# Optimization experiments

Hardware: AMD Instinct MI355X
Metric: run time of the kernel (lower is better)

The kernel has to match this reference:

```python
import jax, jax.numpy as jnp
import numpy as np

D0, D1 = 512, 512          # PSF / sensor dims (DIMS0, DIMS1)
P0, P1 = D0 // 2, D1 // 2  # pad sizes
ITERS = 20
MU1, MU2, MU3 = 1e-6, 1e-5, 1e-5
TAU = 1e-4 * 1000.0        # 0.1, as in module


def _ct(x):  # zero-pad crop-adjoint: sensor -> full size
    return jnp.pad(x, [(0, 0)] * (x.ndim - 2) + [(P0, P0), (P1, P1)])


def _c(x):  # crop full -> sensor size
    return x[..., P0:P0 + D0, P1:P1 + D1]


def _fft2(x):
    return jnp.fft.fft2(x, axes=(-2, -1))


def _ifft2(x):
    return jnp.fft.ifft2(x, axes=(-2, -1))


def _ifftshift(x):
    return jnp.fft.ifftshift(x, axes=(-2, -1))


def _fftshift(x):
    return jnp.fft.fftshift(x, axes=(-2, -1))


def _H(x, Hf):  # forward blur operator
    return jnp.real(_fftshift(_ifft2(Hf * _fft2(_ifftshift(x)))))


def _Hadj(x, Hf):  # adjoint blur operator
    return jnp.real(_fftshift(_ifft2(jnp.conj(Hf) * _fft2(_ifftshift(x)))))


def _psi(x):  # finite differences stacked on last axis -> (..., 2)
    return jnp.stack([jnp.roll(x, 1, axis=-2) - x,
                      jnp.roll(x, 1, axis=-1) - x], axis=-1)


def _psit(u):  # adjoint of _psi
    d0, d1 = u[..., 0], u[..., 1]
    return (jnp.roll(d0, -1, axis=-2) - d0) + (jnp.roll(d1, -1, axis=-1) - d1)


def _soft(v, thresh):
    return jnp.sign(v) * jnp.maximum(jnp.abs(v) - thresh, 0.0)


def _make_ltl():  # FFT of laplacian kernel (Psi^T Psi in Fourier domain)
    lapl = np.zeros((2 * D0, 2 * D1), np.float32)
    lapl[0, 0] = 4.0
    lapl[0, 1] = -1.0
    lapl[1, 0] = -1.0
    lapl[0, -1] = -1.0
    lapl[-1, 0] = -1.0
    return jnp.fft.fft2(jnp.asarray(lapl))


def setup_inputs() -> dict:
    key = jax.random.key(0)
    k1, k2 = jax.random.split(key)
    y = jax.random.uniform(k1, (8, 1, D0, D1), dtype=jnp.float32)
    h = jax.random.uniform(k2, (D0, D1), dtype=jnp.float32)
    return {"y": y, "h": h}


def reference(y, h):
    Hf = _fft2(_ifftshift(_ct(h[None])))            # (1, 2D0, 2D1) complex
    LtL = _make_ltl()                               # (2D0, 2D1) complex
    Vdiv = 1.0 / (_ct(jnp.ones((1, 1, D0, D1), y.dtype)) + MU1)
    Rdiv = 1.0 / (MU1 * jnp.abs(jnp.conj(Hf) * Hf) + MU2 * jnp.abs(LtL) + MU3)
    CTy = _ct(y)                                    # (B,1,2D0,2D1)

    B = y.shape[0]
    full = (B, 1, 2 * D0, 2 * D1)
    X = jnp.zeros(full, y.dtype)
    U = jnp.zeros(full + (2,), y.dtype)
    V = jnp.zeros(full, y.dtype)
    W = jnp.zeros(full, y.dtype)
    a1 = jnp.zeros(full, y.dtype)
    a2 = jnp.zeros(full + (2,), y.dtype)
    a3 = jnp.zeros(full, y.dtype)

    def step(carry, _):
        X, U, V, W, a1, a2, a3 = carry
        U = _soft(_psi(X) + a2 / MU2, TAU / MU2)
        V = Vdiv * (a1 + MU1 * _H(X, Hf) + CTy)
        W = jnp.maximum(a3 / MU3 + X, 0.0)
        r = (MU3 * W - a3) + _psit(MU2 * U - a2) + _Hadj(MU1 * V - a1, Hf)
        X = jnp.real(_fftshift(_ifft2(Rdiv * _fft2(_ifftshift(r)))))
        a1 = a1 + MU1 * (_H(X, Hf) - V)
        a2 = a2 + MU2 * (_psi(X) - U)
        a3 = a3 + MU3 * (X - W)
        return (X, U, V, W, a1, a2, a3), None

    (X, _, _, _, _, _, _), _ = jax.lax.scan(step, (X, U, V, W, a1, a2, a3), None, length=ITERS)
    return _c(X)
```

## Files before the change

kernel.cpp:

```cpp
#include <hip/hip_runtime.h>
#include <math.h>

#define N 1024
#define NN (1024*1024)
#define BATCH 8

static constexpr float MU1 = 1e-6f, MU2 = 1e-5f, MU3 = 1e-5f;

__device__ __forceinline__ float2 cmulf(float2 a, float2 b){
  return make_float2(a.x*b.x - a.y*b.y, a.x*b.y + a.y*b.x);
}
__device__ __forceinline__ float2 conjf(float2 a){ return make_float2(a.x, -a.y); }
__device__ __forceinline__ float softf(float v, float T){
  float a = fmaxf(fabsf(v) - T, 0.f);
  return copysignf(a, v);
}
__device__ __forceinline__ int rev4_10(int p){
  return ((p&3)<<8) | (((p>>2)&3)<<6) | (((p>>4)&3)<<4) | (((p>>6)&3)<<2) | ((p>>8)&3);
}
__device__ __forceinline__ int foldc(int k){
  if (k == 0) return 0;
  if (k == 512) return 1;
  return (k < 512) ? 2*k : 2*(1024-k)+1;
}
__device__ __forceinline__ int unfoldc(int c){
  if (c < 2) return c ? 512 : 0;
  return (c & 1) ? 1024 - ((c-1)>>1) : (c>>1);
}

#define BF4F(x0,x1,x2,x3,u0,u1,u2,u3) { \
  float2 t02p = make_float2((x0).x+(x2).x, (x0).y+(x2).y); \
  float2 t02m = make_float2((x0).x-(x2).x, (x0).y-(x2).y); \
  float2 t13p = make_float2((x1).x+(x3).x, (x1).y+(x3).y); \
  float2 t13m = make_float2((x1).x-(x3).x, (x1).y-(x3).y); \
  u0 = make_float2(t02p.x+t13p.x, t02p.y+t13p.y); \
  u2 = make_float2(t02p.x-t13p.x, t02p.y-t13p.y); \
  u1 = make_float2(t02m.x+t13m.y, t02m.y-t13m.x); \
  u3 = make_float2(t02m.x-t13m.y, t02m.y+t13m.x); }
#define BF4I(x0,x1,x2,x3,u0,u1,u2,u3) { \
  float2 t02p = make_float2((x0).x+(x2).x, (x0).y+(x2).y); \
  float2 t02m = make_float2((x0).x-(x2).x, (x0).y-(x2).y); \
  float2 t13p = make_float2((x1).x+(x3).x, (x1).y+(x3).y); \
  float2 t13m = make_float2((x1).x-(x3).x, (x1).y-(x3).y); \
  u0 = make_float2(t02p.x+t13p.x, t02p.y+t13p.y); \
  u2 = make_float2(t02p.x-t13p.x, t02p.y-t13p.y); \
  u1 = make_float2(t02m.x-t13m.y, t02m.y+t13m.x); \
  u3 = make_float2(t02m.x+t13m.y, t02m.y-t13m.x); }

template<int DIR>
__device__ __forceinline__ void fft1024(float2* bufA, float2* bufB,
                                        const float2* Ws, int tid){
  float2* cur = bufA; float2* oth = bufB;
  int s = 1;
  for (int st = 0; st < 10; ++st){
    int m = 512 >> st;
    #pragma unroll
    for (int bb = 0; bb < 2; ++bb){
      int b = tid + bb*256;
      int p = b >> st;
      int q = b & (s-1);
      float2 a = cur[b];
      float2 c = cur[b + 512];
      float2 w = Ws[b & ~(s-1)];
      if (DIR > 0) w.y = -w.y;
      float2 d = make_float2(a.x - c.x, a.y - c.y);
      oth[q + s*(2*p)]   = make_float2(a.x + c.x, a.y + c.y);
      oth[q + s*(2*p+1)] = cmulf(d, w);
    }
    __syncthreads();
    float2* t = cur; cur = oth; oth = t;
    s <<= 1;
  }
}

__global__ void k_twiddle(float2* W){
  int j = blockIdx.x*blockDim.x + threadIdx.x;
  if (j < 768){
    double a = -2.0 * M_PI * (double)j / 1024.0;
    W[j] = make_float2((float)cos(a), (float)sin(a));
  }
}

__global__ void k_build_h(const float* __restrict__ h, float2* __restrict__ Z){
  int idx = blockIdx.x*256 + threadIdx.x;
  int i = idx >> 10, j = idx & 1023;
  float v = 0.f;
  if (i >= 256 && i < 768 && j >= 256 && j < 768)
    v = h[(i-256)*512 + (j-256)];
  Z[idx] = make_float2(v, 0.f);
}

__global__ void k_filters2(const float2* __restrict__ ZT, float2* __restrict__ HfCb,
                           float* __restrict__ RdCb){
  int id = blockIdx.x*256 + threadIdx.x;
  int blk = id >> 13;
  int rem = id & 8191;
  int p = rem >> 3, c = rem & 7;
  int colp = (blk << 3) | c;
  int ki = rev4_10(p);
  int kj = unfoldc(colp);
  float2 v = ZT[((size_t)kj << 10) | (size_t)ki];
  float sgn = ((ki + kj) & 1) ? -1.f : 1.f;
  HfCb[id] = make_float2(sgn*v.x, sgn*v.y);
  double mag2 = (double)v.x*(double)v.x + (double)v.y*(double)v.y;
  double ltl = 4.0 - 2.0*cos(2.0*M_PI*(double)ki/1024.0)
                   - 2.0*cos(2.0*M_PI*(double)kj/1024.0);
  double rd = 1.0 / ((double)MU1*mag2 + (double)MU2*ltl + (double)MU3);
  RdCb[id] = (float)(rd / ((double)N * (double)N));
}

__global__ void k_init(float* __restrict__ X, float* __restrict__ G1,
                       float* __restrict__ K, float* __restrict__ M,
                       float* __restrict__ G0a, float* __restrict__ G0b,
                       const float* __restrict__ y){
  int idx = blockIdx.x*256 + threadIdx.x;
  int e = idx >> 20, r = (idx >> 10) & 1023, c = idx & 1023;
  X[idx] = 0.f; G1[idx] = 0.f; K[idx] = 0.f; G0a[idx] = 0.f; G0b[idx] = 0.f;
  float m = 0.f;
  if (r >= 256 && r < 768 && c >= 256 && c < 768)
    m = y[(size_t)e*262144 + (size_t)(r-256)*512 + (c-256)] * (MU1/(1.f + MU1));
  M[idx] = m;
}

__global__ __launch_bounds__(256) void k_pA(const float* __restrict__ X,
                                            const float* __restrict__ G0r,
                                            float* __restrict__ G0w,
                                            const float* __restrict__ G1,
                                            const float* __restrict__ K,
                                            const float* __restrict__ M,
                                            float2* __restrict__ Z,
                                            const float2* __restrict__ Wg, int e0){
  __shared__ float2 bufA[N], bufB[N], Ws[512];
  int tid = threadIdx.x;
  int bid = blockIdx.x;
  int i = ((bid & 7) << 7) + (bid >> 3);
  int ce = blockIdx.y, e = e0 + ce;
  size_t eb  = (size_t)e*NN;
  size_t rb  = eb + (size_t)i*N;
  size_t rbm = eb + (size_t)((i-1)&1023)*N;
  size_t rbp = eb + (size_t)((i+1)&1023)*N;
  size_t zb  = (size_t)ce*NN + (size_t)i*N;
  for (int k = tid; k < 512; k += 256) Ws[k] = Wg[k];
  const float T = 1e4f;
  for (int j = tid; j < N; j += 256){
    float xm = X[rbm+j], x = X[rb+j], xp = X[rbp+j];
    float psi0  = xm - x;
    float psi0p = x - xp;
    float g0  = G0r[rb+j], g0p = G0r[rbp+j];
    float u0  = softf(2.f*psi0  - g0 *(1.f/MU2), T);
    float u0p = softf(2.f*psi0p - g0p*(1.f/MU2), T);
    float g0n  = MU2*(u0  - psi0 ) + g0;
    float g0np = MU2*(u0p - psi0p) + g0p;
    G0w[rb+j] = g0n;
    int jp = (j+1) & 1023;
    float s = K[rb+j] + (g0np - g0n) + (G1[rb+jp] - G1[rb+j]);
    bufA[j] = make_float2(s, M[rb+j]);
  }
  __syncthreads();
  fft1024<-1>(bufA, bufB, Ws, tid);
  for (int j = tid; j < N; j += 256) bufB[foldc(j)] = bufA[j];
  __syncthreads();
  for (int j = tid; j < N; j += 256) Z[zb+j] = bufB[j];
}

template<int DIR>
__global__ __launch_bounds__(256) void k_fft_row(float2* Z, const float2* __restrict__ Wg){
  __shared__ float2 bufA[N], bufB[N], Ws[512];
  int tid = threadIdx.x;
  size_t base = ((size_t)blockIdx.y * N + blockIdx.x) * N;
  for (int k = tid; k < 512; k += 256) Ws[k] = Wg[k];
  for (int k = tid; k < N; k += 256) bufA[k] = Z[base + k];
  __syncthreads();
  fft1024<DIR>(bufA, bufB, Ws, tid);
  for (int k = tid; k < N; k += 256) Z[base + k] = bufA[k];
}

__global__ void k_transpose_ip(float2* Z){
  __shared__ float2 ta[32][33], tb[32][33];
  int t = blockIdx.x, ti = 0;
  while (t >= 32 - ti){ t -= 32 - ti; ti++; }
  int tj = ti + t;
  size_t base = (size_t)blockIdx.y * NN;
  int ra = ti*32, ca = tj*32;
  for (int k = threadIdx.y; k < 32; k += 8){
    ta[k][threadIdx.x] = Z[base + (size_t)(ra+k)*N + ca + threadIdx.x];
    if (ti != tj)
      tb[k][threadIdx.x] = Z[base + (size_t)(ca+k)*N + ra + threadIdx.x];
  }
  __syncthreads();
  for (int k = threadIdx.y; k < 32; k += 8){
    Z[base + (size_t)(ra+k)*N + ca + threadIdx.x] = (ti!=tj) ? tb[threadIdx.x][k]
                                                             : ta[threadIdx.x][k];
    if (ti != tj)
      Z[base + (size_t)(ca+k)*N + ra + threadIdx.x] = ta[threadIdx.x][k];
  }
}

#define TADDR(r,c) ((((r)*9) + (c)) ^ (((r) & 16) >> 1))
#define CPV 512
__global__ __launch_bounds__(CPV, 4) void k_colpass(float2* __restrict__ Z,
    const float2* __restrict__ HfCb, const float* __restrict__ RdCb,
    const float2* __restrict__ Wg){
  __shared__ float2 tile[9216];
  __shared__ float2 Ws[768];
  int tid = threadIdx.x;
  int blk = blockIdx.x;
  size_t zbase = (size_t)blockIdx.y*NN + ((size_t)blk<<3);
  for (int k = tid; k < 768; k += CPV) Ws[k] = Wg[k];
  for (int k = tid; k < 8192; k += CPV){
    int r = k >> 3, c = k & 7;
    tile[TADDR(r,c)] = Z[zbase + (size_t)r*N + c];
  }
  __syncthreads();
  {
    int c = tid & 7, j2 = tid >> 3;
    float2 v[4][4];
    #pragma unroll
    for (int a = 0; a < 4; ++a)
      #pragma unroll
      for (int b = 0; b < 4; ++b)
        v[a][b] = tile[TADDR(j2 + 64*b + 256*a, c)];
    #pragma unroll
    for (int b = 0; b < 4; ++b){
      int j1 = j2 + 64*b;
      float2 u0,u1,u2,u3;
      BF4F(v[0][b],v[1][b],v[2][b],v[3][b],u0,u1,u2,u3);
      v[0][b] = u0;
      v[1][b] = cmulf(u1, Ws[j1]);
      v[2][b] = cmulf(u2, Ws[2*j1]);
      v[3][b] = cmulf(u3, Ws[3*j1]);
    }
    int tw = j2 << 2;
    #pragma unroll
    for (int a = 0; a < 4; ++a){
      float2 u0,u1,u2,u3;
      BF4F(v[a][0],v[a][1],v[a][2],v[a][3],u0,u1,u2,u3);
      tile[TADDR(j2 + 256*a, c)]       = u0;
      tile[TADDR(j2 + 64 + 256*a, c)]  = cmulf(u1, Ws[tw]);
      tile[TADDR(j2 + 128 + 256*a, c)] = cmulf(u2, Ws[2*tw]);
      tile[TADDR(j2 + 192 + 256*a, c)] = cmulf(u3, Ws[3*tw]);
    }
  }
  __syncthreads();
  {
    int c = tid & 7, vv = tid >> 3;
    int B2 = vv >> 2, j2 = vv & 3;
    int r0 = 64*B2 + j2;
    float2 v[4][4];
    #pragma unroll
    for (int a = 0; a < 4; ++a)
      #pragma unroll
      for (int b = 0; b < 4; ++b)
        v[a][b] = tile[TADDR(r0 + 4*b + 16*a, c)];
    #pragma unroll
    for (int b = 0; b < 4; ++b){
      int tw = (j2 + 4*b) << 4;
      float2 u0,u1,u2,u3;
      BF4F(v[0][b],v[1][b],v[2][b],v[3][b],u0,u1,u2,u3);
      v[0][b] = u0;
      v[1][b] = cmulf(u1, Ws[tw]);
      v[2][b] = cmulf(u2, Ws[2*tw]);
      v[3][b] = cmulf(u3, Ws[3*tw]);
    }
    int tw3 = j2 << 6;
    #pragma unroll
    for (int a = 0; a < 4; ++a){
      float2 u0,u1,u2,u3;
      BF4F(v[a][0],v[a][1],v[a][2],v[a][3],u0,u1,u2,u3);
      tile[TADDR(r0 + 16*a, c)]      = u0;
      tile[TADDR(r0 + 16*a + 4, c)]  = cmulf(u1, Ws[tw3]);
      tile[TADDR(r0 + 16*a + 8, c)]  = cmulf(u2, Ws[2*tw3]);
      tile[TADDR(r0 + 16*a + 12, c)] = cmulf(u3, Ws[3*tw3]);
    }
  }
  __syncthreads();
  for (int k = tid; k < 2048; k += CPV){
    int c = k & 7, t = k >> 3;
    int r = 4*t;
    float2 x0 = tile[TADDR(r,c)],   x1 = tile[TADDR(r+1,c)];
    float2 x2 = tile[TADDR(r+2,c)], x3 = tile[TADDR(r+3,c)];
    float2 u0,u1,u2,u3;
    BF4F(x0,x1,x2,x3,u0,u1,u2,u3);
    tile[TADDR(r,c)] = u0; tile[TADDR(r+1,c)] = u1;
    tile[TADDR(r+2,c)] = u2; tile[TADDR(r+3,c)] = u3;
  }
  __syncthreads();
  {
    size_t fbase = (size_t)blk << 13;
    for (int k = tid; k < 8192; k += CPV){
      int p = k >> 3, c = k & 7;
      int k1 = rev4_10(p);
      int q = rev4_10((1024 - k1) & 1023);
      int colp = (blk << 3) + c;
      int cm = (colp < 2) ? c : (c ^ 1);
      int pid = (q << 3) | cm;
      if (pid < k) continue;
      float2 Zk = tile[TADDR(p,c)];
      float2 Zr = tile[TADDR(q,cm)];
      float Sre = 0.5f*(Zk.x + Zr.x);
      float Sim = 0.5f*(Zk.y - Zr.y);
      float Mre = 0.5f*(Zk.y + Zr.y);
      float Mim = 0.5f*(Zr.x - Zk.x);
      float2 hf = HfCb[fbase + k];
      float rd  = RdCb[fbase + k];
      float fr = rd*(Sre + hf.x*Mre + hf.y*Mim);
      float fi = rd*(Sim + hf.x*Mim - hf.y*Mre);
      float hr = hf.x*fr - hf.y*fi;
      float hi = hf.x*fi + hf.y*fr;
      tile[TADDR(p,c)] = make_float2(fr - hi, fi + hr);
      if (pid != k) tile[TADDR(q,cm)] = make_float2(fr + hi, hr - fi);
    }
  }
  __syncthreads();
  {
    int c = tid & 7, G = tid >> 3;
    int r0 = 16*G;
    float2 v[4][4];
    #pragma unroll
    for (int a = 0; a < 4; ++a)
      #pragma unroll
      for (int b = 0; b < 4; ++b)
        v[a][b] = tile[TADDR(r0 + 4*a + b, c)];
    #pragma unroll
    for (int a = 0; a < 4; ++a){
      float2 u0,u1,u2,u3;
      BF4I(v[a][0],v[a][1],v[a][2],v[a][3],u0,u1,u2,u3);
      v[a][0]=u0; v[a][1]=u1; v[a][2]=u2; v[a][3]=u3;
    }
    #pragma unroll
    for (int b = 0; b < 4; ++b){
      int tw = b << 6;
      float2 x0 = v[0][b];
      float2 x1 = cmulf(v[1][b], conjf(Ws[tw]));
      float2 x2 = cmulf(v[2][b], conjf(Ws[2*tw]));
      float2 x3 = cmulf(v[3][b], conjf(Ws[3*tw]));
      float2 u0,u1,u2,u3;
      BF4I(x0,x1,x2,x3,u0,u1,u2,u3);
      tile[TADDR(r0 + b, c)]      = u0;
      tile[TADDR(r0 + 4 + b, c)]  = u1;
      tile[TADDR(r0 + 8 + b, c)]  = u2;
      tile[TADDR(r0 + 12 + b, c)] = u3;
    }
  }
  __syncthreads();
  {
    int c = tid & 7, vv = tid >> 3;
    int T3 = vv >> 4, jj = vv & 15;
    int r0 = 256*T3 + jj;
    float2 v[4][4];
    #pragma unroll
    for (int a = 0; a < 4; ++a)
      #pragma unroll
      for (int b = 0; b < 4; ++b)
        v[a][b] = tile[TADDR(r0 + 16*a + 64*b, c)];
    int tw2 = jj << 4;
    #pragma unroll
    for (int b = 0; b < 4; ++b){
      float2 x0 = v[0][b];
      float2 x1 = cmulf(v[1][b], conjf(Ws[tw2]));
      float2 x2 = cmulf(v[2][b], conjf(Ws[2*tw2]));
      float2 x3 = cmulf(v[3][b], conjf(Ws[3*tw2]));
      float2 u0,u1,u2,u3;
      BF4I(x0,x1,x2,x3,u0,u1,u2,u3);
      v[0][b]=u0; v[1][b]=u1; v[2][b]=u2; v[3][b]=u3;
    }
    #pragma unroll
    for (int a = 0; a < 4; ++a){
      int tw = (jj + 16*a) << 2;
      float2 x0 = v[a][0];
      float2 x1 = cmulf(v[a][1], conjf(Ws[tw]));
      float2 x2 = cmulf(v[a][2], conjf(Ws[2*tw]));
      float2 x3 = cmulf(v[a][3], conjf(Ws[3*tw]));
      float2 u0,u1,u2,u3;
      BF4I(x0,x1,x2,x3,u0,u1,u2,u3);
      tile[TADDR(r0 + 16*a, c)]       = u0;
      tile[TADDR(r0 + 16*a + 64, c)]  = u1;
      tile[TADDR(r0 + 16*a + 128, c)] = u2;
      tile[TADDR(r0 + 16*a + 192, c)] = u3;
    }
  }
  __syncthreads();
  for (int k = tid; k < 2048; k += CPV){
    int c = k & 7, t = k >> 3;
    float2 x0 = tile[TADDR(t,c)];
    float2 x1 = cmulf(tile[TADDR(t+256,c)], conjf(Ws[t]));
    float2 x2 = cmulf(tile[TADDR(t+512,c)], conjf(Ws[2*t]));
    float2 x3 = cmulf(tile[TADDR(t+768,c)], conjf(Ws[3*t]));
    float2 u0,u1,u2,u3;
    BF4I(x0,x1,x2,x3,u0,u1,u2,u3);
    tile[TADDR(t,c)] = u0;     tile[TADDR(t+256,c)] = u1;
    tile[TADDR(t+512,c)] = u2; tile[TADDR(t+768,c)] = u3;
  }
  __syncthreads();
  for (int k = tid; k < 8192; k += CPV){
    int r = k >> 3, c = k & 7;
    Z[zbase + (size_t)r*N + c] = tile[TADDR(r,c)];
  }
}

__global__ __launch_bounds__(256) void k_p5(const float2* __restrict__ Z,
                                            float* __restrict__ X, float* __restrict__ K,
                                            float* __restrict__ M, float* __restrict__ G1,
                                            const float* __restrict__ y,
                                            float* __restrict__ out, int writeOut,
                                            const float2* __restrict__ Wg, int e0){
  __shared__ float2 bufA[N], bufB[N], Ws[512];
  int tid = threadIdx.x;
  int i = blockIdx.x, ce = blockIdx.y, e = e0 + ce;
  size_t zb = (size_t)ce*NN + (size_t)i*N;
  size_t sb = (size_t)e*NN + (size_t)i*N;
  for (int k = tid; k < 512; k += 256) Ws[k] = Wg[k];
  for (int k = tid; k < N; k += 256) bufB[k] = Z[zb + k];
  __syncthreads();
  for (int k = tid; k < N; k += 256) bufA[k] = bufB[foldc(k)];
  __syncthreads();
  fft1024<1>(bufA, bufB, Ws, tid);
  bool rcent = (i >= 256 && i < 768);
  const float T = 1e4f;
  for (int j = tid; j < N; j += 256){
    float x = bufA[j].x, hx = bufA[j].y;
    X[sb+j] = x;
    float kk = K[sb+j];
    float w = fmaxf(2.f*x - kk*(1.f/MU3), 0.f);
    K[sb+j] = MU3*(w - x) + kk;
    float m = M[sb+j];
    bool cent = rcent && (j >= 256 && j < 768);
    float cty  = cent ? y[(size_t)e*262144 + (size_t)(i-256)*512 + (j-256)] : 0.f;
    float vdiv = cent ? (1.f/(1.f + MU1)) : (1.f/MU1);
    float v = vdiv*(2.f*MU1*hx - m + cty);
    M[sb+j] = MU1*(v - hx) + m;
    float xm = bufA[(j-1)&1023].x;
    float psi1 = xm - x;
    float g1 = G1[sb+j];
    float u1 = softf(2.f*psi1 - g1*(1.f/MU2), T);
    G1[sb+j] = MU2*(u1 - psi1) + g1;
    if (writeOut && cent)
      out[(size_t)e*262144 + (size_t)(i-256)*512 + (j-256)] = x;
  }
}

__global__ void k_crop(const float* __restrict__ X, float* __restrict__ out){
  int t = blockIdx.x*256 + threadIdx.x;
  int e = t >> 18;
  int r = (t >> 9) & 511;
  int c = t & 511;
  out[t] = X[(size_t)e*NN + (size_t)(r+256)*N + (c+256)];
}

extern "C" void kernel_launch(void* const* d_in, const int* in_sizes, int n_in,
                              void* d_out, int out_size, void* d_ws, size_t ws_size,
                              hipStream_t stream){
  const float* y = (const float*)d_in[0];
  const float* h = (const float*)d_in[1];
  float* out = (float*)d_out;

  size_t fplane = (size_t)BATCH * NN;
  float* X   = (float*)d_ws;
  float* G1  = X   + fplane;
  float* K   = G1  + fplane;
  float* M   = K   + fplane;
  float* G0a = M   + fplane;
  float* G0b = G0a + fplane;
  float2* HfCb = (float2*)(G0b + fplane);
  float*  RdCb = (float*)(HfCb + NN);
  float2* Wtab = (float2*)(RdCb + NN);
  float2* Zws  = Wtab + 768;
  size_t used = (size_t)((char*)Zws - (char*)d_ws);

  int CH = 0;
  for (int c = BATCH; c >= 1; c >>= 1)
    if (used + (size_t)c * NN * sizeof(float2) <= ws_size){ CH = c; break; }
  bool fallback = (CH == 0);
  float2* Z = fallback ? (float2*)d_out : Zws;
  if (CH == 0) CH = 1;

  k_twiddle<<<3, 256, 0, stream>>>(Wtab);
  k_build_h<<<NN/256, 256, 0, stream>>>(h, Z);
  k_fft_row<-1><<<dim3(N,1), 256, 0, stream>>>(Z, Wtab);
  k_transpose_ip<<<dim3(528,1), dim3(32,8), 0, stream>>>(Z);
  k_fft_row<-1><<<dim3(N,1), 256, 0, stream>>>(Z, Wtab);
  k_filters2<<<NN/256, 256, 0, stream>>>(Z, HfCb, RdCb);
  k_init<<<BATCH*NN/256, 256, 0, stream>>>(X, G1, K, M, G0a, G0b, y);

  for (int t = 0; t < 20; ++t){
    const float* G0r = (t & 1) ? G0b : G0a;
    float*       G0w = (t & 1) ? G0a : G0b;
    int wo = (t == 19 && !fallback) ? 1 : 0;
    for (int e0 = 0; e0 < BATCH; e0 += CH){
      k_pA<<<dim3(N,CH), 256, 0, stream>>>(X, G0r, G0w, G1, K, M, Z, Wtab, e0);
      k_colpass<<<dim3(128,CH), CPV, 0, stream>>>(Z, HfCb, RdCb, Wtab);
      k_p5<<<dim3(N,CH), 256, 0, stream>>>(Z, X, K, M, G1, y, out, wo, Wtab, e0);
    }
  }
  if (fallback)
    k_crop<<<(BATCH*512*512)/256, 256, 0, stream>>>(X, out);
}
```

Measured before the change: 3.769 ms.

## Use radix-4 row FFTs, on-chip twiddles and Rdiv, skip init pass

Replaces the radix-2 ping-pong row FFTs in the forward and final passes with in-place radix-4 FFTs on a padded shared buffer. Twiddles are now generated on-chip with sincosf instead of loaded from a table, and the Rdiv filter is recomputed in the column pass rather than read from memory. The zero-init kernel is removed by special-casing the first iterations, and Z can spill into the output buffer so all 8 batch elements fit in one chunk. Together these cut memory traffic, kernel launches and FFT passes, at the cost of extra ALU work and float-precision twiddles and filter values.

```diff
diff --git a/kernel.cpp b/kernel.cpp
--- a/kernel.cpp
+++ b/kernel.cpp
@@ -26,6 +26,9 @@
 __device__ __forceinline__ int unfoldc(int c){
   if (c < 2) return c ? 512 : 0;
   return (c & 1) ? 1024 - ((c-1)>>1) : (c>>1);
+}
+__device__ __forceinline__ float2* ZP(float2* Zw, float2* Zd, int ce){
+  return (ce == 7) ? Zd : (Zw + (size_t)ce * NN);
 }
 
 #define BF4F(x0,x1,x2,x3,u0,u1,u2,u3) { \
@@ -47,6 +50,15 @@
   u1 = make_float2(t02m.x-t13m.y, t02m.y+t13m.x); \
   u3 = make_float2(t02m.x+t13m.y, t02m.y-t13m.x); }
 
+__device__ __forceinline__ void genWs(float2* Ws, int cnt, int tid, int nthr){
+  for (int j = tid; j < cnt; j += nthr){
+    double a = (double)j * (-M_PI / 512.0);
+    float s, c;
+    sincosf((float)a, &s, &c);
+    Ws[j] = make_float2(c, s);
+  }
+}
+
 template<int DIR>
 __device__ __forceinline__ void fft1024(float2* bufA, float2* bufB,
                                         const float2* Ws, int tid){
@@ -73,11 +85,44 @@
   }
 }
 
-__global__ void k_twiddle(float2* W){
-  int j = blockIdx.x*blockDim.x + threadIdx.x;
-  if (j < 768){
-    double a = -2.0 * M_PI * (double)j / 1024.0;
-    W[j] = make_float2((float)cos(a), (float)sin(a));
+#define A1(p) ((p) + ((p)>>4))
+
+__device__ __forceinline__ void fwd_r4_row(float2* t4, const float2* Ws, int tid){
+  #pragma unroll
+  for (int s = 0; s < 5; ++s){
+    int log2L = 8 - 2*s;
+    int L = 1 << log2L;
+    int j = tid & (L-1);
+    int base = ((tid >> log2L) << (log2L+2)) + j;
+    int tw = j << (2*s);
+    float2 x0 = t4[A1(base)],     x1 = t4[A1(base+L)],
+           x2 = t4[A1(base+2*L)], x3 = t4[A1(base+3*L)];
+    float2 u0,u1,u2,u3;
+    BF4F(x0,x1,x2,x3,u0,u1,u2,u3);
+    t4[A1(base)]     = u0;
+    t4[A1(base+L)]   = cmulf(u1, Ws[tw]);
+    t4[A1(base+2*L)] = cmulf(u2, Ws[2*tw]);
+    t4[A1(base+3*L)] = cmulf(u3, Ws[3*tw]);
+    __syncthreads();
+  }
+}
+
+__device__ __forceinline__ void inv_r4_row(float2* t4, const float2* Ws, int tid){
+  #pragma unroll
+  for (int s = 0; s < 5; ++s){
+    int H = 1 << (2*s);
+    int j = tid & (H-1);
+    int base = ((tid >> (2*s)) << (2*s+2)) + j;
+    int tw = j << (8 - 2*s);
+    float2 x0 = t4[A1(base)];
+    float2 x1 = cmulf(t4[A1(base+H)],   conjf(Ws[tw]));
+    float2 x2 = cmulf(t4[A1(base+2*H)], conjf(Ws[2*tw]));
+    float2 x3 = cmulf(t4[A1(base+3*H)], conjf(Ws[3*tw]));
+    float2 u0,u1,u2,u3;
+    BF4I(x0,x1,x2,x3,u0,u1,u2,u3);
+    t4[A1(base)] = u0;     t4[A1(base+H)] = u1;
+    t4[A1(base+2*H)] = u2; t4[A1(base+3*H)] = u3;
+    __syncthreads();
   }
 }
 
@@ -90,85 +135,12 @@
   Z[idx] = make_float2(v, 0.f);
 }
 
-__global__ void k_filters2(const float2* __restrict__ ZT, float2* __restrict__ HfCb,
-                           float* __restrict__ RdCb){
-  int id = blockIdx.x*256 + threadIdx.x;
-  int blk = id >> 13;
-  int rem = id & 8191;
-  int p = rem >> 3, c = rem & 7;
-  int colp = (blk << 3) | c;
-  int ki = rev4_10(p);
-  int kj = unfoldc(colp);
-  float2 v = ZT[((size_t)kj << 10) | (size_t)ki];
-  float sgn = ((ki + kj) & 1) ? -1.f : 1.f;
-  HfCb[id] = make_float2(sgn*v.x, sgn*v.y);
-  double mag2 = (double)v.x*(double)v.x + (double)v.y*(double)v.y;
-  double ltl = 4.0 - 2.0*cos(2.0*M_PI*(double)ki/1024.0)
-                   - 2.0*cos(2.0*M_PI*(double)kj/1024.0);
-  double rd = 1.0 / ((double)MU1*mag2 + (double)MU2*ltl + (double)MU3);
-  RdCb[id] = (float)(rd / ((double)N * (double)N));
-}
-
-__global__ void k_init(float* __restrict__ X, float* __restrict__ G1,
-                       float* __restrict__ K, float* __restrict__ M,
-                       float* __restrict__ G0a, float* __restrict__ G0b,
-                       const float* __restrict__ y){
-  int idx = blockIdx.x*256 + threadIdx.x;
-  int e = idx >> 20, r = (idx >> 10) & 1023, c = idx & 1023;
-  X[idx] = 0.f; G1[idx] = 0.f; K[idx] = 0.f; G0a[idx] = 0.f; G0b[idx] = 0.f;
-  float m = 0.f;
-  if (r >= 256 && r < 768 && c >= 256 && c < 768)
-    m = y[(size_t)e*262144 + (size_t)(r-256)*512 + (c-256)] * (MU1/(1.f + MU1));
-  M[idx] = m;
-}
-
-__global__ __launch_bounds__(256) void k_pA(const float* __restrict__ X,
-                                            const float* __restrict__ G0r,
-                                            float* __restrict__ G0w,
-                                            const float* __restrict__ G1,
-                                            const float* __restrict__ K,
-                                            const float* __restrict__ M,
-                                            float2* __restrict__ Z,
-                                            const float2* __restrict__ Wg, int e0){
-  __shared__ float2 bufA[N], bufB[N], Ws[512];
-  int tid = threadIdx.x;
-  int bid = blockIdx.x;
-  int i = ((bid & 7) << 7) + (bid >> 3);
-  int ce = blockIdx.y, e = e0 + ce;
-  size_t eb  = (size_t)e*NN;
-  size_t rb  = eb + (size_t)i*N;
-  size_t rbm = eb + (size_t)((i-1)&1023)*N;
-  size_t rbp = eb + (size_t)((i+1)&1023)*N;
-  size_t zb  = (size_t)ce*NN + (size_t)i*N;
-  for (int k = tid; k < 512; k += 256) Ws[k] = Wg[k];
-  const float T = 1e4f;
-  for (int j = tid; j < N; j += 256){
-    float xm = X[rbm+j], x = X[rb+j], xp = X[rbp+j];
-    float psi0  = xm - x;
-    float psi0p = x - xp;
-    float g0  = G0r[rb+j], g0p = G0r[rbp+j];
-    float u0  = softf(2.f*psi0  - g0 *(1.f/MU2), T);
-    float u0p = softf(2.f*psi0p - g0p*(1.f/MU2), T);
-    float g0n  = MU2*(u0  - psi0 ) + g0;
-    float g0np = MU2*(u0p - psi0p) + g0p;
-    G0w[rb+j] = g0n;
-    int jp = (j+1) & 1023;
-    float s = K[rb+j] + (g0np - g0n) + (G1[rb+jp] - G1[rb+j]);
-    bufA[j] = make_float2(s, M[rb+j]);
-  }
-  __syncthreads();
-  fft1024<-1>(bufA, bufB, Ws, tid);
-  for (int j = tid; j < N; j += 256) bufB[foldc(j)] = bufA[j];
-  __syncthreads();
-  for (int j = tid; j < N; j += 256) Z[zb+j] = bufB[j];
-}
-
 template<int DIR>
-__global__ __launch_bounds__(256) void k_fft_row(float2* Z, const float2* __restrict__ Wg){
+__global__ __launch_bounds__(256) void k_fft_row(float2* Z){
   __shared__ float2 bufA[N], bufB[N], Ws[512];
   int tid = threadIdx.x;
   size_t base = ((size_t)blockIdx.y * N + blockIdx.x) * N;
-  for (int k = tid; k < 512; k += 256) Ws[k] = Wg[k];
+  genWs(Ws, 512, tid, 256);
   for (int k = tid; k < N; k += 256) bufA[k] = Z[base + k];
   __syncthreads();
   fft1024<DIR>(bufA, bufB, Ws, tid);
@@ -196,20 +168,87 @@
   }
 }
 
+__global__ void k_filters2(const float2* __restrict__ ZT, float2* __restrict__ HfCb){
+  int id = blockIdx.x*256 + threadIdx.x;
+  int blk = id >> 13;
+  int rem = id & 8191;
+  int p = rem >> 3, c = rem & 7;
+  int colp = (blk << 3) | c;
+  int ki = rev4_10(p);
+  int kj = unfoldc(colp);
+  float2 v = ZT[((size_t)kj << 10) | (size_t)ki];
+  float sgn = ((ki + kj) & 1) ? -1.f : 1.f;
+  HfCb[id] = make_float2(sgn*v.x, sgn*v.y);
+}
+
+__global__ __launch_bounds__(256) void k_pA(const float* __restrict__ X,
+                                            const float* __restrict__ G0r,
+                                            float* __restrict__ G0w,
+                                            const float* __restrict__ G1,
+                                            const float* __restrict__ K,
+                                            const float* __restrict__ M,
+                                            const float* __restrict__ y,
+                                            float2* __restrict__ Zw,
+                                            float2* __restrict__ Zd,
+                                            int e0, int mode){
+  __shared__ float2 t4[1088], Ws[768];
+  int tid = threadIdx.x;
+  int bid = blockIdx.x;
+  int i = ((bid & 7) << 7) + (bid >> 3);
+  int ce = blockIdx.y, e = e0 + ce;
+  size_t eb  = (size_t)e*NN;
+  size_t rb  = eb + (size_t)i*N;
+  size_t rbm = eb + (size_t)((i-1)&1023)*N;
+  size_t rbp = eb + (size_t)((i+1)&1023)*N;
+  float2* Zp = ZP(Zw, Zd, ce);
+  size_t zb  = (size_t)i*N;
+  genWs(Ws, 768, tid, 256);
+  const float T = 1e4f;
+  if (mode == 2){
+    bool rcent = (i >= 256 && i < 768);
+    for (int j = tid; j < N; j += 256){
+      float m0 = 0.f;
+      if (rcent && j >= 256 && j < 768)
+        m0 = y[(size_t)e*262144 + (size_t)(i-256)*512 + (j-256)] * (MU1/(1.f + MU1));
+      t4[A1(j)] = make_float2(0.f, m0);
+    }
+  } else {
+    for (int j = tid; j < N; j += 256){
+      float xm = X[rbm+j], x = X[rb+j], xp = X[rbp+j];
+      float psi0  = xm - x;
+      float psi0p = x - xp;
+      float g0  = (mode == 1) ? 0.f : G0r[rb+j];
+      float g0p = (mode == 1) ? 0.f : G0r[rbp+j];
+      float u0  = softf(2.f*psi0  - g0 *(1.f/MU2), T);
+      float u0p = softf(2.f*psi0p - g0p*(1.f/MU2), T);
+      float g0n  = MU2*(u0  - psi0 ) + g0;
+      float g0np = MU2*(u0p - psi0p) + g0p;
+      G0w[rb+j] = g0n;
+      int jp = (j+1) & 1023;
+      float s = K[rb+j] + (g0np - g0n) + (G1[rb+jp] - G1[rb+j]);
+      t4[A1(j)] = make_float2(s, M[rb+j]);
+    }
+  }
+  __syncthreads();
+  fwd_r4_row(t4, Ws, tid);
+  for (int c = tid; c < N; c += 256)
+    Zp[zb + c] = t4[A1(rev4_10(unfoldc(c)))];
+}
+
 #define TADDR(r,c) ((((r)*9) + (c)) ^ (((r) & 16) >> 1))
 #define CPV 512
-__global__ __launch_bounds__(CPV, 4) void k_colpass(float2* __restrict__ Z,
-    const float2* __restrict__ HfCb, const float* __restrict__ RdCb,
-    const float2* __restrict__ Wg){
+__global__ __launch_bounds__(CPV) void k_colpass(float2* __restrict__ Zw,
+    float2* __restrict__ Zd, const float2* __restrict__ HfCb){
   __shared__ float2 tile[9216];
   __shared__ float2 Ws[768];
   int tid = threadIdx.x;
   int blk = blockIdx.x;
-  size_t zbase = (size_t)blockIdx.y*NN + ((size_t)blk<<3);
-  for (int k = tid; k < 768; k += CPV) Ws[k] = Wg[k];
+  float2* Zp = ZP(Zw, Zd, blockIdx.y);
+  size_t zbase = (size_t)(blk<<3);
+  genWs(Ws, 768, tid, CPV);
   for (int k = tid; k < 8192; k += CPV){
     int r = k >> 3, c = k & 7;
-    tile[TADDR(r,c)] = Z[zbase + (size_t)r*N + c];
+    tile[TADDR(r,c)] = Zp[zbase + (size_t)r*N + c];
   }
   __syncthreads();
   {
@@ -302,7 +341,12 @@
       float Mre = 0.5f*(Zk.y + Zr.y);
       float Mim = 0.5f*(Zr.x - Zk.x);
       float2 hf = HfCb[fbase + k];
-      float rd  = RdCb[fbase + k];
+      int kj = unfoldc(colp);
+      float cA = Ws[(k1 < 768) ? k1 : 1024 - k1].x;
+      float cB = Ws[(kj < 768) ? kj : 1024 - kj].x;
+      float ltl = 4.f - 2.f*cA - 2.f*cB;
+      float mag2 = hf.x*hf.x + hf.y*hf.y;
+      float rd = 9.5367431640625e-7f / (MU1*mag2 + MU2*ltl + MU3);
       float fr = rd*(Sre + hf.x*Mre + hf.y*Mim);
       float fi = rd*(Sim + hf.x*Mim - hf.y*Mre);
       float hr = hf.x*fr - hf.y*fi;
@@ -394,44 +438,47 @@
   __syncthreads();
   for (int k = tid; k < 8192; k += CPV){
     int r = k >> 3, c = k & 7;
-    Z[zbase + (size_t)r*N + c] = tile[TADDR(r,c)];
-  }
-}
-
-__global__ __launch_bounds__(256) void k_p5(const float2* __restrict__ Z,
+    Zp[zbase + (size_t)r*N + c] = tile[TADDR(r,c)];
+  }
+}
+
+__global__ __launch_bounds__(256) void k_p5(float2* __restrict__ Zw,
+                                            float2* __restrict__ Zd,
                                             float* __restrict__ X, float* __restrict__ K,
                                             float* __restrict__ M, float* __restrict__ G1,
                                             const float* __restrict__ y,
                                             float* __restrict__ out, int writeOut,
-                                            const float2* __restrict__ Wg, int e0){
-  __shared__ float2 bufA[N], bufB[N], Ws[512];
+                                            int e0, int first){
+  __shared__ float2 t4[1088], bufZ[N], Ws[768];
   int tid = threadIdx.x;
   int i = blockIdx.x, ce = blockIdx.y, e = e0 + ce;
-  size_t zb = (size_t)ce*NN + (size_t)i*N;
+  float2* Zp = ZP(Zw, Zd, ce);
+  size_t zb = (size_t)i*N;
   size_t sb = (size_t)e*NN + (size_t)i*N;
-  for (int k = tid; k < 512; k += 256) Ws[k] = Wg[k];
-  for (int k = tid; k < N; k += 256) bufB[k] = Z[zb + k];
-  __syncthreads();
-  for (int k = tid; k < N; k += 256) bufA[k] = bufB[foldc(k)];
-  __syncthreads();
-  fft1024<1>(bufA, bufB, Ws, tid);
+  genWs(Ws, 768, tid, 256);
+  for (int k = tid; k < N; k += 256) bufZ[k] = Zp[zb + k];
+  __syncthreads();
+  for (int p = tid; p < N; p += 256) t4[A1(p)] = bufZ[foldc(rev4_10(p))];
+  __syncthreads();
+  inv_r4_row(t4, Ws, tid);
   bool rcent = (i >= 256 && i < 768);
   const float T = 1e4f;
   for (int j = tid; j < N; j += 256){
-    float x = bufA[j].x, hx = bufA[j].y;
+    float2 xv = t4[A1(j)];
+    float x = xv.x, hx = xv.y;
     X[sb+j] = x;
-    float kk = K[sb+j];
+    bool cent = rcent && (j >= 256 && j < 768);
+    float cty  = cent ? y[(size_t)e*262144 + (size_t)(i-256)*512 + (j-256)] : 0.f;
+    float kk = first ? 0.f : K[sb+j];
     float w = fmaxf(2.f*x - kk*(1.f/MU3), 0.f);
     K[sb+j] = MU3*(w - x) + kk;
-    float m = M[sb+j];
-    bool cent = rcent && (j >= 256 && j < 768);
-    float cty  = cent ? y[(size_t)e*262144 + (size_t)(i-256)*512 + (j-256)] : 0.f;
+    float m = first ? (cent ? cty*(MU1/(1.f+MU1)) : 0.f) : M[sb+j];
     float vdiv = cent ? (1.f/(1.f + MU1)) : (1.f/MU1);
     float v = vdiv*(2.f*MU1*hx - m + cty);
     M[sb+j] = MU1*(v - hx) + m;
-    float xm = bufA[(j-1)&1023].x;
+    float xm = t4[A1((j-1)&1023)].x;
     float psi1 = xm - x;
-    float g1 = G1[sb+j];
+    float g1 = first ? 0.f : G1[sb+j];
     float u1 = softf(2.f*psi1 - g1*(1.f/MU2), T);
     G1[sb+j] = MU2*(u1 - psi1) + g1;
     if (writeOut && cent)
@@ -462,36 +509,35 @@
   float* G0a = M   + fplane;
   float* G0b = G0a + fplane;
   float2* HfCb = (float2*)(G0b + fplane);
-  float*  RdCb = (float*)(HfCb + NN);
-  float2* Wtab = (float2*)(RdCb + NN);
-  float2* Zws  = Wtab + 768;
-  size_t used = (size_t)((char*)Zws - (char*)d_ws);
-
-  int CH = 0;
-  for (int c = BATCH; c >= 1; c >>= 1)
-    if (used + (size_t)c * NN * sizeof(float2) <= ws_size){ CH = c; break; }
-  bool fallback = (CH == 0);
-  float2* Z = fallback ? (float2*)d_out : Zws;
-  if (CH == 0) CH = 1;
-
-  k_twiddle<<<3, 256, 0, stream>>>(Wtab);
-  k_build_h<<<NN/256, 256, 0, stream>>>(h, Z);
-  k_fft_row<-1><<<dim3(N,1), 256, 0, stream>>>(Z, Wtab);
-  k_transpose_ip<<<dim3(528,1), dim3(32,8), 0, stream>>>(Z);
-  k_fft_row<-1><<<dim3(N,1), 256, 0, stream>>>(Z, Wtab);
-  k_filters2<<<NN/256, 256, 0, stream>>>(Z, HfCb, RdCb);
-  k_init<<<BATCH*NN/256, 256, 0, stream>>>(X, G1, K, M, G0a, G0b, y);
+  float2* Zw   = HfCb + NN;
+  size_t used = (size_t)((char*)Zw - (char*)d_ws);
+  size_t zcap = (ws_size > used) ? (ws_size - used) / ((size_t)NN * sizeof(float2)) : 0;
+
+  int CH; float2* Zd; bool needCrop;
+  if (zcap >= 8){       CH = 8; Zd = Zw + 7*(size_t)NN; needCrop = true; }
+  else if (zcap == 7){  CH = 8; Zd = (float2*)d_out;    needCrop = true; }
+  else if (zcap >= 4){  CH = 4; Zd = Zw; needCrop = false; }
+  else if (zcap >= 2){  CH = 2; Zd = Zw; needCrop = false; }
+  else if (zcap >= 1){  CH = 1; Zd = Zw; needCrop = false; }
+  else {                CH = 1; Zw = (float2*)d_out; Zd = Zw; needCrop = true; }
+
+  k_build_h<<<NN/256, 256, 0, stream>>>(h, Zw);
+  k_fft_row<-1><<<dim3(N,1), 256, 0, stream>>>(Zw);
+  k_transpose_ip<<<dim3(528,1), dim3(32,8), 0, stream>>>(Zw);
+  k_fft_row<-1><<<dim3(N,1), 256, 0, stream>>>(Zw);
+  k_filters2<<<NN/256, 256, 0, stream>>>(Zw, HfCb);
 
   for (int t = 0; t < 20; ++t){
     const float* G0r = (t & 1) ? G0b : G0a;
     float*       G0w = (t & 1) ? G0a : G0b;
-    int wo = (t == 19 && !fallback) ? 1 : 0;
+    int mode = (t == 0) ? 2 : ((t == 1) ? 1 : 0);
+    int wo = (t == 19 && !needCrop) ? 1 : 0;
     for (int e0 = 0; e0 < BATCH; e0 += CH){
-      k_pA<<<dim3(N,CH), 256, 0, stream>>>(X, G0r, G0w, G1, K, M, Z, Wtab, e0);
-      k_colpass<<<dim3(128,CH), CPV, 0, stream>>>(Z, HfCb, RdCb, Wtab);
-      k_p5<<<dim3(N,CH), 256, 0, stream>>>(Z, X, K, M, G1, y, out, wo, Wtab, e0);
-    }
-  }
-  if (fallback)
+      k_pA<<<dim3(N,CH), 256, 0, stream>>>(X, G0r, G0w, G1, K, M, y, Zw, Zd, e0, mode);
+      k_colpass<<<dim3(128,CH), CPV, 0, stream>>>(Zw, Zd, HfCb);
+      k_p5<<<dim3(N,CH), 256, 0, stream>>>(Zw, Zd, X, K, M, G1, y, out, wo, e0, (t==0)?1:0);
+    }
+  }
+  if (needCrop)
     k_crop<<<(BATCH*512*512)/256, 256, 0, stream>>>(X, out);
 }
```

After: 3.444 ms. 1.09x faster.
